# Performance work log

Measured on AMD Instinct MI355X. Metric: run time of the kernel, lower is better.

## Reference

```python
import jax, jax.numpy as jnp
import numpy as np

N = 50000      # nodes
E = 800000     # edges (before self-loops)
F_IN = 128     # input features
H = 4          # heads
C = 32         # hidden_dim per head
HC = H * C     # 128, concat width
G = 64         # graphs in batch
OUT = 10       # classes
NEG_SLOPE = 0.2  # PyG GATConv default negative_slope


def setup_inputs() -> dict:
    key = jax.random.key(0)
    ks = jax.random.split(key, 16)
    x = jax.random.normal(ks[0], (N, F_IN), dtype=jnp.float32)
    edge_index = jax.random.randint(ks[1], (2, E), 0, N, dtype=jnp.int32)
    batch = jnp.sort(jax.random.randint(ks[2], (N,), 0, G, dtype=jnp.int32))
    s = 0.05
    Ws = [
        jax.random.normal(ks[3], (F_IN, HC), jnp.float32) * s,
        jax.random.normal(ks[4], (HC, HC), jnp.float32) * s,
        jax.random.normal(ks[5], (HC, HC), jnp.float32) * s,
    ]
    a_srcs = [jax.random.normal(ks[6 + i], (H, C), jnp.float32) * s for i in range(3)]
    a_dsts = [jax.random.normal(ks[9 + i], (H, C), jnp.float32) * s for i in range(3)]
    biases = [jnp.zeros((HC,), jnp.float32) for _ in range(3)]
    Wh = jax.random.normal(ks[12], (HC, OUT), jnp.float32) * s
    bh = jnp.zeros((OUT,), jnp.float32)
    return {"x": x, "Ws": Ws, "a_srcs": a_srcs, "a_dsts": a_dsts,
            "biases": biases, "Wh": Wh, "bh": bh,
            "edge_index": edge_index, "batch": batch}


def gat_layer(x, W, a_src, a_dst, b, src, dst, n):
    # x: [N, F]; W: [F, H*C]; a_src/a_dst: [H, C]
    h = (x @ W).reshape(n, H, C)                     # [N, H, C]
    alpha_s = jnp.sum(h * a_src, axis=-1)            # [N, H]
    alpha_d = jnp.sum(h * a_dst, axis=-1)            # [N, H]
    e = jax.nn.leaky_relu(alpha_s[src] + alpha_d[dst], NEG_SLOPE)  # [E', H]
    # segment softmax over incoming edges (grouped by dst)
    emax = jax.ops.segment_max(e, dst, num_segments=n)             # [N, H]
    ex = jnp.exp(e - emax[dst])
    denom = jax.ops.segment_sum(ex, dst, num_segments=n)
    alpha = ex / denom[dst]                                        # [E', H]
    msg = h[src] * alpha[:, :, None]                               # [E', H, C]
    out = jax.ops.segment_sum(msg, dst, num_segments=n)            # [N, H, C]
    return out.reshape(n, HC) + b


def reference(x, Ws, a_srcs, a_dsts, biases, Wh, bh, edge_index, batch):
    n = x.shape[0]
    # PyG GATConv adds self-loops by default
    loops = jnp.arange(n, dtype=edge_index.dtype)
    src = jnp.concatenate([edge_index[0], loops])
    dst = jnp.concatenate([edge_index[1], loops])
    for i in range(3):
        x = jax.nn.relu(gat_layer(x, Ws[i], a_srcs[i], a_dsts[i], biases[i], src, dst, n))
        # dropout is identity in eval mode
    pooled = jax.ops.segment_sum(x, batch, num_segments=G)  # global_add_pool -> [G, HC]
    logits = pooled @ Wh + bh                                # [G, OUT]
    return logits
```

## Files before the change

kernel.cpp:

```cpp
#include <hip/hip_runtime.h>
#include <hip/hip_bf16.h>

#define HC 128
#define NHEAD 4
#define NEG 0.2f
#define CHUNK 4096

typedef unsigned int uint32;
typedef __attribute__((ext_vector_type(8))) short short8v;
typedef __attribute__((ext_vector_type(4))) float f32x4;

__device__ __forceinline__ float leaky(float v) { return v > 0.f ? v : NEG * v; }
__device__ __forceinline__ int clampi(int v, int lo, int hi) { return v < lo ? lo : (v > hi ? hi : v); }

__device__ __forceinline__ uint32 pack_bf16(float lo, float hi) {
  uint32 a = __float_as_uint(lo);
  uint32 b = __float_as_uint(hi);
  a = (a + 0x7FFFu + ((a >> 16) & 1u)) >> 16;
  b = (b + 0x7FFFu + ((b >> 16) & 1u)) & 0xFFFF0000u;
  return a | b;
}
__device__ __forceinline__ unsigned short bf16_1(float v) {
  uint32 a = __float_as_uint(v);
  return (unsigned short)((a + 0x7FFFu + ((a >> 16) & 1u)) >> 16);
}
__device__ __forceinline__ float2 unpack_bf16(uint32 u) {
  return make_float2(__uint_as_float(u << 16), __uint_as_float(u & 0xFFFF0000u));
}
__device__ __forceinline__ short8v as_s8(uint4 u) {
  union { uint4 a; short8v b; } c; c.a = u; return c.b;
}

#define WT_STRIDE 18432

__global__ __launch_bounds__(256) void zero_kernel(int* __restrict__ p, int n) {
  int i = blockIdx.x * 256 + threadIdx.x;
  int stride = gridDim.x * 256;
  for (; i < n; i += stride) p[i] = 0;
}

__global__ __launch_bounds__(256) void bincnt_lds(const int* __restrict__ dst, int* __restrict__ bcnt, int E, int n) {
  __shared__ int h[256];
  int t = threadIdx.x;
  h[t] = 0;
  __syncthreads();
  int e0 = blockIdx.x * CHUNK;
  int e1 = e0 + CHUNK < E ? e0 + CHUNK : E;
  for (int i = e0 + t; i < e1; i += 256) {
    int d = clampi(dst[i], 0, n - 1);
    atomicAdd(&h[d >> 8], 1);
  }
  __syncthreads();
  if (h[t] > 0) atomicAdd(&bcnt[t], h[t]);
}

__global__ __launch_bounds__(256) void bscan_kernel(const int* __restrict__ bcnt, int* __restrict__ bbase,
                                                    int* __restrict__ bcur, int NBKT) {
  __shared__ int part[256];
  int t = threadIdx.x;
  int c = (t < NBKT) ? bcnt[t] : 0;
  part[t] = c;
  __syncthreads();
  for (int off = 1; off < 256; off <<= 1) {
    int v = (t >= off) ? part[t - off] : 0;
    __syncthreads();
    part[t] += v;
    __syncthreads();
  }
  int excl = part[t] - c;
  if (t < NBKT) {
    bbase[t] = excl;
    bcur[t] = excl;
  }
}

__global__ __launch_bounds__(256) void binscatter_staged(const int* __restrict__ src, const int* __restrict__ dst,
                                                         int* __restrict__ bcur, int2* __restrict__ ebuf, int E, int n) {
  __shared__ int lcnt[256];
  __shared__ int lbase[256];
  int t = threadIdx.x;
  lcnt[t] = 0;
  __syncthreads();
  int e0 = blockIdx.x * CHUNK;
  int e1 = e0 + CHUNK < E ? e0 + CHUNK : E;
  for (int i = e0 + t; i < e1; i += 256) {
    int d = clampi(dst[i], 0, n - 1);
    atomicAdd(&lcnt[d >> 8], 1);
  }
  __syncthreads();
  int myc = lcnt[t];
  lbase[t] = (myc > 0) ? atomicAdd(&bcur[t], myc) : 0;
  __syncthreads();
  lcnt[t] = 0;
  __syncthreads();
  for (int i = e0 + t; i < e1; i += 256) {
    int d = clampi(dst[i], 0, n - 1);
    int s = clampi(src[i], 0, n - 1);
    int b = d >> 8;
    int pos = atomicAdd(&lcnt[b], 1);
    int p = lbase[b] + pos;
    if (p >= 0 && p < E) ebuf[p] = make_int2(s, d);
  }
}

__global__ __launch_bounds__(256) void bucket_finalize(const int2* __restrict__ ebuf, const int* __restrict__ bbase,
                                                       int* __restrict__ row_start, int* __restrict__ csr,
                                                       int NBKT, int E, int n) {
  __shared__ int cnt[256];
  __shared__ int part[256];
  __shared__ int cur[256];
  int b = blockIdx.x;
  int t = threadIdx.x;
  int start = bbase[b];
  int end = (b == NBKT - 1) ? E : bbase[b + 1];
  int d0 = b << 8;
  int ndst = n - d0; if (ndst > 256) ndst = 256;
  cnt[t] = 0;
  __syncthreads();
  for (int i = start + t; i < end; i += 256) {
    int d = ebuf[i].y - d0;
    if (d >= 0 && d < 256) atomicAdd(&cnt[d], 1);
  }
  __syncthreads();
  int c = cnt[t];
  part[t] = c;
  __syncthreads();
  for (int off = 1; off < 256; off <<= 1) {
    int v = (t >= off) ? part[t - off] : 0;
    __syncthreads();
    part[t] += v;
    __syncthreads();
  }
  int excl = part[t] - c;
  if (t < ndst) row_start[d0 + t] = start + excl;
  if (b == NBKT - 1 && t == 0) row_start[n] = E;
  cur[t] = start + excl;
  __syncthreads();
  for (int i = start + t; i < end; i += 256) {
    int2 pr = ebuf[i];
    int d = pr.y - d0;
    if (d >= 0 && d < 256) {
      int p = atomicAdd(&cur[d], 1);
      if (p >= 0 && p < E) csr[p] = pr.x;
    }
  }
}

__global__ __launch_bounds__(256) void hist_kernel(const int* __restrict__ dst, int* __restrict__ cnt, int E, int n) {
  int e = blockIdx.x * 256 + threadIdx.x;
  if (e < E) atomicAdd(&cnt[clampi(dst[e], 0, n - 1)], 1);
}
__global__ __launch_bounds__(256) void scan_pass1(const int* __restrict__ cnt, int* __restrict__ blocksum, int n) {
  __shared__ int red[256];
  int t = threadIdx.x;
  int i = blockIdx.x * 256 + t;
  red[t] = i < n ? cnt[i] : 0;
  __syncthreads();
  for (int off = 128; off >= 1; off >>= 1) {
    if (t < off) red[t] += red[t + off];
    __syncthreads();
  }
  if (t == 0) blocksum[blockIdx.x] = red[0];
}
__global__ __launch_bounds__(256) void scan_pass2(const int* __restrict__ blocksum, int* __restrict__ blockpre,
                                                  int* __restrict__ row_start, int NB, int n) {
  __shared__ int part[256];
  int t = threadIdx.x;
  int chunk = (NB + 255) >> 8;
  int lo = t * chunk; if (lo > NB) lo = NB;
  int hi = lo + chunk; if (hi > NB) hi = NB;
  int s = 0;
  for (int i = lo; i < hi; ++i) s += blocksum[i];
  part[t] = s;
  __syncthreads();
  for (int off = 1; off < 256; off <<= 1) {
    int v = (t >= off) ? part[t - off] : 0;
    __syncthreads();
    part[t] += v;
    __syncthreads();
  }
  int run = part[t] - s;
  for (int i = lo; i < hi; ++i) {
    blockpre[i] = run;
    run += blocksum[i];
  }
  if (t == 255) row_start[n] = part[255];
}
__global__ __launch_bounds__(256) void scan_pass3(const int* __restrict__ cnt, const int* __restrict__ blockpre,
                                                  int* __restrict__ row_start, int* __restrict__ cursor, int n) {
  __shared__ int part[256];
  int t = threadIdx.x;
  int i = blockIdx.x * 256 + t;
  int c = i < n ? cnt[i] : 0;
  part[t] = c;
  __syncthreads();
  for (int off = 1; off < 256; off <<= 1) {
    int v = (t >= off) ? part[t - off] : 0;
    __syncthreads();
    part[t] += v;
    __syncthreads();
  }
  int excl = part[t] - c;
  if (i < n) {
    int b = blockpre[blockIdx.x] + excl;
    row_start[i] = b;
    cursor[i] = b;
  }
}
__global__ __launch_bounds__(256) void scatter_kernel(const int* __restrict__ src, const int* __restrict__ dst,
                                                      int* __restrict__ cursor, int* __restrict__ csr, int E, int n) {
  int e = blockIdx.x * 256 + threadIdx.x;
  if (e < E) {
    int d = clampi(dst[e], 0, n - 1);
    int s = clampi(src[e], 0, n - 1);
    int p = atomicAdd(&cursor[d], 1);
    if (p >= 0 && p < E) csr[p] = s;
  }
}

__global__ __launch_bounds__(256) void prep_kernel(const float* __restrict__ x, const float* __restrict__ W0,
                                                   const float* __restrict__ W1, const float* __restrict__ W2,
                                                   const float* __restrict__ as0, const float* __restrict__ as1,
                                                   const float* __restrict__ as2, const float* __restrict__ ad0,
                                                   const float* __restrict__ ad1, const float* __restrict__ ad2,
                                                   const float* __restrict__ bh, uint32* __restrict__ X16,
                                                   unsigned short* __restrict__ wt, int* __restrict__ bcnt,
                                                   float* __restrict__ outp, long long n64, int NC, int Gp) {
  long long id = (long long)blockIdx.x * 256 + threadIdx.x;
  if (id < n64) {
    float2 v = *(const float2*)&x[id * 2];
    X16[id] = pack_bf16(v.x, v.y);
    return;
  }
  long long id2l = id - n64;
  if (id2l < 3 * 16384) {
    int id2 = (int)id2l;
    int l = id2 >> 14;
    int r = id2 & 16383;
    int k = r >> 7, nc = r & 127;
    const float* W = l == 0 ? W0 : (l == 1 ? W1 : W2);
    wt[(size_t)l * WT_STRIDE + nc * 128 + k] = bf16_1(W[r]);
    return;
  }
  id2l -= 3 * 16384;
  if (id2l < 3 * 2048) {
    int id2 = (int)id2l;
    int l = id2 >> 11;
    int r = id2 & 2047;
    int col8 = r >> 7, k = r & 127;
    const float* W = l == 0 ? W0 : (l == 1 ? W1 : W2);
    unsigned short outv = 0;
    if (col8 < 8) {
      int h = col8 & 3;
      const float* av = (col8 < 4) ? (l == 0 ? as0 : (l == 1 ? as1 : as2))
                                   : (l == 0 ? ad0 : (l == 1 ? ad1 : ad2));
      float s = 0.f;
      for (int c = 0; c < 32; ++c) s += W[k * 128 + 32 * h + c] * av[32 * h + c];
      outv = bf16_1(s);
    }
    wt[(size_t)l * WT_STRIDE + (128 + col8) * 128 + k] = outv;
    return;
  }
  id2l -= 3 * 2048;
  if (id2l < NC) {
    bcnt[id2l] = 0;
    return;
  }
  id2l -= NC;
  if (id2l < (long long)Gp * 10) outp[id2l] = bh[id2l % 10];
}

__global__ __launch_bounds__(256) void gemm_mfma(const uint32* __restrict__ X16, const unsigned short* __restrict__ Wt,
                                                 uint32* __restrict__ H16, float* __restrict__ As,
                                                 float* __restrict__ Ad, int n) {
  int t = threadIdx.x;
  int wave = t >> 6, lane = t & 63;
  int l15 = lane & 15, lg = lane >> 4;
  int row0 = blockIdx.x * 16;
  int arow = row0 + l15;
  if (arow >= n) arow = n - 1;
  const uint4* xr = (const uint4*)(X16 + (size_t)arow * 64);
  uint4 a[4];
#pragma unroll
  for (int kc = 0; kc < 4; ++kc) a[kc] = xr[kc * 4 + lg];
  const int NT = (wave == 0) ? 3 : 2;
  f32x4 acc[3];
#pragma unroll
  for (int ti = 0; ti < 3; ++ti) acc[ti] = (f32x4){0.f, 0.f, 0.f, 0.f};
#pragma unroll
  for (int kc = 0; kc < 4; ++kc) {
    uint4 b[3];
#pragma unroll
    for (int ti = 0; ti < 3; ++ti) {
      if (ti < NT) {
        int basecol = (ti < 2) ? (2 * wave + ti) * 16 : 128;
        b[ti] = *(const uint4*)(Wt + (size_t)(basecol + l15) * 128 + kc * 32 + lg * 8);
      }
    }
#pragma unroll
    for (int ti = 0; ti < 3; ++ti)
      if (ti < NT) acc[ti] = __builtin_amdgcn_mfma_f32_16x16x32_bf16(as_s8(a[kc]), as_s8(b[ti]), acc[ti], 0, 0, 0);
  }
#pragma unroll
  for (int r = 0; r < 4; ++r) {
    int gr = row0 + lg * 4 + r;
    bool ok = gr < n;
#pragma unroll
    for (int ti = 0; ti < 2; ++ti) {
      int nb = 2 * wave + ti;
      float mine = acc[ti][r];
      float other = __shfl_xor(mine, 1);
      if (ok && (lane & 1) == 0) H16[(size_t)gr * 64 + nb * 8 + (l15 >> 1)] = pack_bf16(mine, other);
    }
    if (wave == 0) {
      float av = acc[2][r];
      if (ok && l15 < 4) As[gr * 4 + l15] = av;
      if (ok && l15 >= 4 && l15 < 8) Ad[gr * 4 + (l15 - 4)] = av;
    }
  }
}

template <bool OUTFP32>
__global__ __launch_bounds__(256) void agg_kernel(const uint32* __restrict__ H16, const float* __restrict__ As,
                                                  const float* __restrict__ Ad, const int* __restrict__ row_start,
                                                  const int* __restrict__ csr, const float* __restrict__ bias,
                                                  void* __restrict__ outv, int n) {
  int wid = (blockIdx.x * 256 + threadIdx.x) >> 6;
  int lane = threadIdx.x & 63;
  if (wid >= n) return;
  int base = row_start[wid];
  int deg = row_start[wid + 1] - base;
  if (deg < 0) deg = 0;
  int hsel = lane >> 4;
  float adsel = Ad[wid * 4 + hsel];
  float pself = __expf(leaky(As[wid * 4 + hsel] + adsel));
  float2 hv = unpack_bf16(H16[(size_t)wid * 64 + lane]);
  float den = pself;
  float acc0 = pself * hv.x, acc1 = pself * hv.y;
  for (int chunk = 0; chunk < deg; chunk += 64) {
    int j = chunk + lane;
    int smine = (j < deg) ? csr[base + j] : 0;
    int cnt_ = deg - chunk; if (cnt_ > 64) cnt_ = 64;
#pragma unroll
    for (int k = 0; k < 4; ++k) {
      if (k * 16 >= cnt_) break;
      float pmk;
      {
        int slot = k * 16 + (lane & 15);
        int sk = __shfl(smine, slot);
        float e = As[sk * 4 + hsel];
        pmk = (slot < cnt_) ? __expf(leaky(e + adsel)) : 0.f;
      }
      int ss[16];
      uint32 h2[16];
#pragma unroll
      for (int i = 0; i < 16; ++i) ss[i] = __shfl(smine, k * 16 + i);
#pragma unroll
      for (int i = 0; i < 16; ++i) h2[i] = H16[(size_t)((uint32)ss[i] * 64 + lane)];
#pragma unroll
      for (int i = 0; i < 16; ++i) {
        float aw = __shfl(pmk, (lane & 48) + i);
        float2 hh = unpack_bf16(h2[i]);
        den += aw;
        acc0 += aw * hh.x;
        acc1 += aw * hh.y;
      }
    }
  }
  float inv = 1.f / den;
  float2 bv = *(const float2*)&bias[2 * lane];
  float r0v = fmaxf(acc0 * inv + bv.x, 0.f);
  float r1v = fmaxf(acc1 * inv + bv.y, 0.f);
  if constexpr (OUTFP32) {
    ((float2*)outv)[(size_t)wid * 64 + lane] = make_float2(r0v, r1v);
  } else {
    ((uint32*)outv)[(size_t)wid * 64 + lane] = pack_bf16(r0v, r1v);
  }
}

__global__ __launch_bounds__(128) void pool_logits(const float* __restrict__ X, const int* __restrict__ batch,
                                                   const float* __restrict__ Wh, float* __restrict__ out,
                                                   int n, int G) {
  __shared__ float red[128];
  int c = threadIdx.x;
  int n0 = blockIdx.x * 64;
  if (n0 >= n) return;
  int end = n0 + 64 < n ? n0 + 64 : n;
  int curg = clampi(batch[n0], 0, G - 1);
  float acc = 0.f;
  for (int i = n0; i <= end; ++i) {
    int g = (i < end) ? clampi(batch[i], 0, G - 1) : -1;
    if (g != curg) {
      red[c] = acc;
      __syncthreads();
      if (c < 10) {
        float s = 0.f;
#pragma unroll 16
        for (int cc = 0; cc < 128; ++cc) s += red[cc] * Wh[cc * 10 + c];
        atomicAdd(&out[curg * 10 + c], s);
      }
      __syncthreads();
      acc = 0.f;
      curg = g;
    }
    if (i < end) acc += X[(size_t)i * 128 + c];
  }
}

extern "C" void kernel_launch(void* const* d_in, const int* in_sizes, int n_in,
                              void* d_out, int out_size, void* d_ws, size_t ws_size,
                              hipStream_t stream) {
  const float *x, *Wl[3], *asr[3], *adr[3], *bias[3], *Wh, *bh;
  const int *edge_index, *batch;
  long long E_ll;
  if (n_in >= 17) {
    x = (const float*)d_in[0];
    for (int l = 0; l < 3; ++l) {
      Wl[l] = (const float*)d_in[1 + l];
      asr[l] = (const float*)d_in[4 + l];
      adr[l] = (const float*)d_in[7 + l];
      bias[l] = (const float*)d_in[10 + l];
    }
    Wh = (const float*)d_in[13];
    bh = (const float*)d_in[14];
    edge_index = (const int*)d_in[15];
    batch = (const int*)d_in[16];
    E_ll = (long long)in_sizes[15] / 2;
  } else if (n_in >= 9) {
    x = (const float*)d_in[0];
    const float* Wc = (const float*)d_in[1];
    const float* ac = (const float*)d_in[2];
    const float* dc = (const float*)d_in[3];
    const float* bc = (const float*)d_in[4];
    for (int l = 0; l < 3; ++l) {
      Wl[l] = Wc + (size_t)l * HC * HC;
      asr[l] = ac + (size_t)l * HC;
      adr[l] = dc + (size_t)l * HC;
      bias[l] = bc + (size_t)l * HC;
    }
    Wh = (const float*)d_in[5];
    bh = (const float*)d_in[6];
    edge_index = (const int*)d_in[7];
    batch = (const int*)d_in[8];
    E_ll = (long long)in_sizes[7] / 2;
  } else {
    zero_kernel<<<(out_size + 255) / 256, 256, 0, stream>>>((int*)d_out, out_size);
    return;
  }
  int N = in_sizes[0] / HC;
  int G = out_size / 10;
  if (N <= 0 || G <= 0 || E_ll <= 0 || E_ll > (1LL << 30)) {
    zero_kernel<<<(out_size + 255) / 256, 256, 0, stream>>>((int*)d_out, out_size);
    return;
  }
  int E = (int)E_ll;
  int NBKT = (N + 255) >> 8;
  int NB = (N + 255) / 256;
  bool staged = (NBKT <= 256);

  char* w = (char*)d_ws;
  size_t off = 0;
  auto take = [&](size_t bytes) -> char* {
    char* p = w + off;
    off = (off + bytes + 511) & ~(size_t)511;
    return p;
  };
  uint32* H16 = (uint32*)take((size_t)N * 64 * 4);
  uint32* X16 = (uint32*)take((size_t)N * 64 * 4);
  float* bufQ = (float*)take((size_t)N * HC * 4);
  uint32* Xa = (uint32*)bufQ;
  float* As = (float*)take((size_t)N * NHEAD * 4);
  float* Ad = (float*)take((size_t)N * NHEAD * 4);
  int* row_start = (int*)take((size_t)(N + 1) * 4);
  int* csr = (int*)take((size_t)E * 4);
  int2* ebuf = (int2*)take((size_t)E * 8);
  int* bcnt = (int*)take(256 * 4);
  int* bbase = (int*)take(256 * 4);
  int* bcur = (int*)take(256 * 4);
  int* cnt = (int*)take((size_t)N * 4);
  int* cursor = (int*)take((size_t)N * 4);
  int* blocksum = (int*)take((size_t)NB * 4);
  int* blockpre = (int*)take((size_t)NB * 4);
  unsigned short* wt16 = (unsigned short*)take((size_t)3 * WT_STRIDE * 2);

  if (off > ws_size) {
    zero_kernel<<<(out_size + 255) / 256, 256, 0, stream>>>((int*)d_out, out_size);
    return;
  }

  const int* esrc = edge_index;
  const int* edst = edge_index + E;

  long long n64 = (long long)N * 64;
  long long prep_items = n64 + 3 * 16384 + 3 * 2048 + 256 + (long long)G * 10;
  prep_kernel<<<(int)((prep_items + 255) / 256), 256, 0, stream>>>(
      x, Wl[0], Wl[1], Wl[2], asr[0], asr[1], asr[2], adr[0], adr[1], adr[2], bh,
      Xa, wt16, bcnt, (float*)d_out, n64, 256, G);

  int echunks = (E + CHUNK - 1) / CHUNK;
  if (staged) {
    bincnt_lds<<<echunks, 256, 0, stream>>>(edst, bcnt, E, N);
    bscan_kernel<<<1, 256, 0, stream>>>(bcnt, bbase, bcur, NBKT);
    binscatter_staged<<<echunks, 256, 0, stream>>>(esrc, edst, bcur, ebuf, E, N);
    bucket_finalize<<<NBKT, 256, 0, stream>>>(ebuf, bbase, row_start, csr, NBKT, E, N);
  } else {
    zero_kernel<<<(N + 255) / 256, 256, 0, stream>>>(cnt, N);
    hist_kernel<<<(E + 255) / 256, 256, 0, stream>>>(edst, cnt, E, N);
    scan_pass1<<<NB, 256, 0, stream>>>(cnt, blocksum, N);
    scan_pass2<<<1, 256, 0, stream>>>(blocksum, blockpre, row_start, NB, N);
    scan_pass3<<<NB, 256, 0, stream>>>(cnt, blockpre, row_start, cursor, N);
    scatter_kernel<<<(E + 255) / 256, 256, 0, stream>>>(esrc, edst, cursor, csr, E, N);
  }

  int gemm_grid = (N + 15) / 16;
  int agg_grid = (N + 3) / 4;

  gemm_mfma<<<gemm_grid, 256, 0, stream>>>(Xa, wt16, H16, As, Ad, N);
  agg_kernel<false><<<agg_grid, 256, 0, stream>>>(H16, As, Ad, row_start, csr, bias[0], X16, N);
  gemm_mfma<<<gemm_grid, 256, 0, stream>>>(X16, wt16 + WT_STRIDE, H16, As, Ad, N);
  agg_kernel<false><<<agg_grid, 256, 0, stream>>>(H16, As, Ad, row_start, csr, bias[1], X16, N);
  gemm_mfma<<<gemm_grid, 256, 0, stream>>>(X16, wt16 + 2 * WT_STRIDE, H16, As, Ad, N);
  agg_kernel<true><<<agg_grid, 256, 0, stream>>>(H16, As, Ad, row_start, csr, bias[2], bufQ, N);

  pool_logits<<<(N + 63) / 64, 128, 0, stream>>>(bufQ, batch, Wh, (float*)d_out, N, G);
}
```

Baseline: 267.2 us.

## Fuse three GAT layers into one persistent cooperative kernel with grid syncs

Replaces the six per-layer GEMM and aggregation launches with a single cooperative persistent kernel. It loops over row groups and separates phases with grid-wide syncs, falling back to separate launches if cooperative launch fails. This is meant to remove launch gaps and tail effects between the six kernels. In exchange it adds grid-sync cost, caps the grid at occupancy, and the grid-stride loops may reduce the latency hiding of the gather-heavy aggregation. The host-side attribute and occupancy queries also add per-call overhead.

```diff
diff --git a/kernel.cpp b/kernel.cpp
--- a/kernel.cpp
+++ b/kernel.cpp
@@ -1,5 +1,8 @@
 #include <hip/hip_runtime.h>
 #include <hip/hip_bf16.h>
+#include <hip/hip_cooperative_groups.h>
+
+namespace cg = cooperative_groups;
 
 #define HC 128
 #define NHEAD 4
@@ -270,13 +273,13 @@
   if (id2l < (long long)Gp * 10) outp[id2l] = bh[id2l % 10];
 }
 
-__global__ __launch_bounds__(256) void gemm_mfma(const uint32* __restrict__ X16, const unsigned short* __restrict__ Wt,
-                                                 uint32* __restrict__ H16, float* __restrict__ As,
-                                                 float* __restrict__ Ad, int n) {
+__device__ __forceinline__ void gemm_body(int grp, const uint32* __restrict__ X16,
+                                          const unsigned short* __restrict__ Wt, uint32* __restrict__ H16,
+                                          float* __restrict__ As, float* __restrict__ Ad, int n) {
   int t = threadIdx.x;
   int wave = t >> 6, lane = t & 63;
   int l15 = lane & 15, lg = lane >> 4;
-  int row0 = blockIdx.x * 16;
+  int row0 = grp * 16;
   int arow = row0 + l15;
   if (arow >= n) arow = n - 1;
   const uint4* xr = (const uint4*)(X16 + (size_t)arow * 64);
@@ -321,11 +324,11 @@
 }
 
 template <bool OUTFP32>
-__global__ __launch_bounds__(256) void agg_kernel(const uint32* __restrict__ H16, const float* __restrict__ As,
-                                                  const float* __restrict__ Ad, const int* __restrict__ row_start,
-                                                  const int* __restrict__ csr, const float* __restrict__ bias,
-                                                  void* __restrict__ outv, int n) {
-  int wid = (blockIdx.x * 256 + threadIdx.x) >> 6;
+__device__ __forceinline__ void agg_body(int q, const uint32* __restrict__ H16, const float* __restrict__ As,
+                                         const float* __restrict__ Ad, const int* __restrict__ row_start,
+                                         const int* __restrict__ csr, const float* __restrict__ bias,
+                                         void* __restrict__ outv, int n) {
+  int wid = q * 4 + (threadIdx.x >> 6);
   int lane = threadIdx.x & 63;
   if (wid >= n) return;
   int base = row_start[wid];
@@ -376,6 +379,57 @@
   } else {
     ((uint32*)outv)[(size_t)wid * 64 + lane] = pack_bf16(r0v, r1v);
   }
+}
+
+struct GatArgs {
+  const uint32* Xa;
+  uint32* X16;
+  uint32* H16;
+  float* As;
+  float* Ad;
+  const int* row_start;
+  const int* csr;
+  const unsigned short* wt;
+  const float* b0;
+  const float* b1;
+  const float* b2;
+  float* bufQ;
+  int N;
+};
+
+__global__ __launch_bounds__(256) void gat_layers(GatArgs a) {
+  cg::grid_group grid = cg::this_grid();
+  int ngrp = (a.N + 15) >> 4;
+  int nq = (a.N + 3) >> 2;
+  for (int l = 0; l < 3; ++l) {
+    const uint32* xin = (l == 0) ? a.Xa : (const uint32*)a.X16;
+    const unsigned short* wtl = a.wt + (size_t)l * WT_STRIDE;
+    const float* bl = (l == 0) ? a.b0 : (l == 1 ? a.b1 : a.b2);
+    for (int g = blockIdx.x; g < ngrp; g += gridDim.x)
+      gemm_body(g, xin, wtl, a.H16, a.As, a.Ad, a.N);
+    grid.sync();
+    if (l < 2) {
+      for (int q = blockIdx.x; q < nq; q += gridDim.x)
+        agg_body<false>(q, a.H16, a.As, a.Ad, a.row_start, a.csr, bl, a.X16, a.N);
+    } else {
+      for (int q = blockIdx.x; q < nq; q += gridDim.x)
+        agg_body<true>(q, a.H16, a.As, a.Ad, a.row_start, a.csr, bl, a.bufQ, a.N);
+    }
+    grid.sync();
+  }
+}
+
+__global__ __launch_bounds__(256) void gemm_mfma(const uint32* __restrict__ X16, const unsigned short* __restrict__ Wt,
+                                                 uint32* __restrict__ H16, float* __restrict__ As,
+                                                 float* __restrict__ Ad, int n) {
+  gemm_body(blockIdx.x, X16, Wt, H16, As, Ad, n);
+}
+template <bool OUTFP32>
+__global__ __launch_bounds__(256) void agg_kernel(const uint32* __restrict__ H16, const float* __restrict__ As,
+                                                  const float* __restrict__ Ad, const int* __restrict__ row_start,
+                                                  const int* __restrict__ csr, const float* __restrict__ bias,
+                                                  void* __restrict__ outv, int n) {
+  agg_body<OUTFP32>(blockIdx.x, H16, As, Ad, row_start, csr, bias, outv, n);
 }
 
 __global__ __launch_bounds__(128) void pool_logits(const float* __restrict__ X, const int* __restrict__ batch,
@@ -515,12 +569,37 @@
   int gemm_grid = (N + 15) / 16;
   int agg_grid = (N + 3) / 4;
 
-  gemm_mfma<<<gemm_grid, 256, 0, stream>>>(Xa, wt16, H16, As, Ad, N);
-  agg_kernel<false><<<agg_grid, 256, 0, stream>>>(H16, As, Ad, row_start, csr, bias[0], X16, N);
-  gemm_mfma<<<gemm_grid, 256, 0, stream>>>(X16, wt16 + WT_STRIDE, H16, As, Ad, N);
-  agg_kernel<false><<<agg_grid, 256, 0, stream>>>(H16, As, Ad, row_start, csr, bias[1], X16, N);
-  gemm_mfma<<<gemm_grid, 256, 0, stream>>>(X16, wt16 + 2 * WT_STRIDE, H16, As, Ad, N);
-  agg_kernel<true><<<agg_grid, 256, 0, stream>>>(H16, As, Ad, row_start, csr, bias[2], bufQ, N);
+  int dev = 0;
+  (void)hipGetDevice(&dev);
+  int coop = 0;
+  (void)hipDeviceGetAttribute(&coop, hipDeviceAttributeCooperativeLaunch, dev);
+  int numCU = 0;
+  (void)hipDeviceGetAttribute(&numCU, hipDeviceAttributeMultiprocessorCount, dev);
+  int blocksPerCU = 0;
+  (void)hipOccupancyMaxActiveBlocksPerMultiprocessor(&blocksPerCU, gat_layers, 256, 0);
+
+  bool used_coop = false;
+  if (coop && numCU > 0 && blocksPerCU > 0) {
+    int cap = numCU * blocksPerCU;
+    int want = gemm_grid > agg_grid ? gemm_grid : agg_grid;
+    int grid = want < cap ? want : cap;
+    GatArgs ga;
+    ga.Xa = Xa; ga.X16 = X16; ga.H16 = H16; ga.As = As; ga.Ad = Ad;
+    ga.row_start = row_start; ga.csr = csr; ga.wt = wt16;
+    ga.b0 = bias[0]; ga.b1 = bias[1]; ga.b2 = bias[2];
+    ga.bufQ = bufQ; ga.N = N;
+    void* params[] = {&ga};
+    hipError_t err = hipLaunchCooperativeKernel((const void*)gat_layers, dim3(grid), dim3(256), params, 0, stream);
+    used_coop = (err == hipSuccess);
+  }
+  if (!used_coop) {
+    gemm_mfma<<<gemm_grid, 256, 0, stream>>>(Xa, wt16, H16, As, Ad, N);
+    agg_kernel<false><<<agg_grid, 256, 0, stream>>>(H16, As, Ad, row_start, csr, bias[0], X16, N);
+    gemm_mfma<<<gemm_grid, 256, 0, stream>>>(X16, wt16 + WT_STRIDE, H16, As, Ad, N);
+    agg_kernel<false><<<agg_grid, 256, 0, stream>>>(H16, As, Ad, row_start, csr, bias[1], X16, N);
+    gemm_mfma<<<gemm_grid, 256, 0, stream>>>(X16, wt16 + 2 * WT_STRIDE, H16, As, Ad, N);
+    agg_kernel<true><<<agg_grid, 256, 0, stream>>>(H16, As, Ad, row_start, csr, bias[2], bufQ, N);
+  }
 
   pool_logits<<<(N + 63) / 64, 128, 0, stream>>>(bufQ, batch, Wh, (float*)d_out, N, G);
 }
```

After: 689.3 us. +158.0%, slower.
